# Kernel tuning notes

Hardware: AMD Instinct MI355X
Metric: run time of the kernel (lower is better)

The kernel has to match this reference:

```python
import jax, jax.numpy as jnp
import numpy as np

B, L, EMB, U, V = 128, 64, 512, 1024, 50257
BN_EPS = 0.001


def setup_inputs() -> dict:
    key = jax.random.key(0)
    ks = jax.random.split(key, 20)
    s = 0.02
    return {
        "x": jax.random.randint(ks[0], (B, 1), 0, V, dtype=jnp.int64),
        "features": jax.random.normal(ks[1], (B, L, EMB), jnp.float32),
        "hidden": jax.random.normal(ks[2], (1, B, U), jnp.float32),
        "emb_table": jax.random.normal(ks[3], (V, EMB), jnp.float32) * s,
        "Uattn_w": jax.random.normal(ks[4], (U, EMB), jnp.float32) * s,
        "Uattn_b": jnp.zeros((U,), jnp.float32),
        "Wattn_w": jax.random.normal(ks[5], (U, U), jnp.float32) * s,
        "Wattn_b": jnp.zeros((U,), jnp.float32),
        "Vattn_w": jax.random.normal(ks[6], (1, U), jnp.float32) * s,
        "Vattn_b": jnp.zeros((1,), jnp.float32),
        "W_ih": jax.random.normal(ks[7], (3 * U, U), jnp.float32) * s,
        "W_hh": jax.random.normal(ks[8], (3 * U, U), jnp.float32) * s,
        "b_ih": jnp.zeros((3 * U,), jnp.float32),
        "b_hh": jnp.zeros((3 * U,), jnp.float32),
        "fc_w": jax.random.normal(ks[9], (U, U), jnp.float32) * s,
        "fc_b": jnp.zeros((U,), jnp.float32),
        "bn_gamma": jnp.ones((U,), jnp.float32),
        "bn_beta": jnp.zeros((U,), jnp.float32),
        "bn_mean": jnp.zeros((U,), jnp.float32),
        "bn_var": jnp.ones((U,), jnp.float32),
        "fc2_w": jax.random.normal(ks[10], (V, U), jnp.float32) * s,
        "fc2_b": jnp.zeros((V,), jnp.float32),
    }


def reference(x, features, hidden, emb_table, Uattn_w, Uattn_b, Wattn_w, Wattn_b,
              Vattn_w, Vattn_b, W_ih, W_hh, b_ih, b_hh, fc_w, fc_b,
              bn_gamma, bn_beta, bn_mean, bn_var, fc2_w, fc2_b):
    h = hidden[0]  # [B, U]
    # Bahdanau attention
    Uf = jnp.einsum('ble,ue->blu', features, Uattn_w) + Uattn_b        # [B,L,U]
    Wh = h @ Wattn_w.T + Wattn_b                                        # [B,U]
    score = jnp.tanh(Uf + Wh[:, None, :]) @ Vattn_w.T + Vattn_b        # [B,L,1]
    attn = jax.nn.softmax(score, axis=1)                                # [B,L,1]
    ctx = jnp.sum(attn * features, axis=1)                              # [B,EMB]
    # embed token and concat -> GRU input (seq len 1)
    e = emb_table[x[:, 0]]                                              # [B,EMB]
    gin = jnp.concatenate([ctx, e], axis=-1)                            # [B,U]
    # single-step GRU (PyTorch gate convention)
    gi = gin @ W_ih.T + b_ih                                            # [B,3U]
    gh = h @ W_hh.T + b_hh                                              # [B,3U]
    i_r, i_z, i_n = jnp.split(gi, 3, axis=-1)
    h_r, h_z, h_n = jnp.split(gh, 3, axis=-1)
    r = jax.nn.sigmoid(i_r + h_r)
    z = jax.nn.sigmoid(i_z + h_z)
    n = jnp.tanh(i_n + r * h_n)
    h_new = (1.0 - z) * n + z * h                                       # [B,U]
    # head: fc -> (dropout: identity in eval) -> BN (eval) -> fc2
    y = h_new @ fc_w.T + fc_b
    y = (y - bn_mean) * jax.lax.rsqrt(bn_var + BN_EPS) * bn_gamma + bn_beta
    logits = y @ fc2_w.T + fc2_b                                        # [B,V]
    return logits, h_new[None, :, :], attn
```

## Files before the change

### kernel.cpp

```cpp
#include <hip/hip_runtime.h>

typedef short bf8 __attribute__((ext_vector_type(8)));
typedef float f32x4 __attribute__((ext_vector_type(4)));

__device__ inline short f2bfs(float f) {
    unsigned u = __builtin_bit_cast(unsigned, f);
    u += 0x7FFFu + ((u >> 16) & 1u);
    return (short)(u >> 16);
}

__device__ inline unsigned pk2(float x, float y) {
    return (unsigned)(unsigned short)f2bfs(x) |
           ((unsigned)(unsigned short)f2bfs(y) << 16);
}

__device__ inline float bf2f(short s) {
    unsigned u = ((unsigned)(unsigned short)s) << 16;
    return __builtin_bit_cast(float, u);
}

__device__ inline bf8 cvt_frag(f32x4 lo, f32x4 hi) {
    union { bf8 v; unsigned u[4]; } r;
    r.u[0] = pk2(lo[0], lo[1]);
    r.u[1] = pk2(lo[2], lo[3]);
    r.u[2] = pk2(hi[0], hi[1]);
    r.u[3] = pk2(hi[2], hi[3]);
    return r.v;
}

__device__ inline void gl_lds16(const void* g, void* l) {
    __builtin_amdgcn_global_load_lds(
        (const __attribute__((address_space(1))) unsigned int*)g,
        (__attribute__((address_space(3))) unsigned int*)l,
        16, 0, 0);
}

#define BAR() asm volatile("s_barrier" ::: "memory")

template<int N> __device__ __forceinline__ void waitvm() {
    if constexpr (N == 8)      asm volatile("s_waitcnt vmcnt(8)"  ::: "memory");
    else if constexpr (N == 6) asm volatile("s_waitcnt vmcnt(6)"  ::: "memory");
    else if constexpr (N == 4) asm volatile("s_waitcnt vmcnt(4)"  ::: "memory");
    else if constexpr (N == 3) asm volatile("s_waitcnt vmcnt(3)"  ::: "memory");
    else                       asm volatile("s_waitcnt vmcnt(0)"  ::: "memory");
}

#define MFMA16 __builtin_amdgcn_mfma_f32_16x16x32_bf16

template<int EPI, int BM_, bool OBF>
__device__ __forceinline__ void gemm_body(
    char* smem,
    const short* __restrict__ A, const float* __restrict__ W,
    const float* __restrict__ bias, void* __restrict__ Cv,
    int N, int K, int lda, int n0, int m0,
    const float* __restrict__ q0, const float* __restrict__ q1,
    const float* __restrict__ q2, const float* __restrict__ q3,
    float* __restrict__ score)
{
    constexpr int FM  = BM_ / 32;
    constexpr int ATS = BM_ * 64;
    constexpr int LPT = (BM_ == 128) ? 4 : 3;

    const int lane = threadIdx.x & 63;
    const int wave = threadIdx.x >> 6;
    const int wm0  = (wave >> 1) * (BM_ / 2);
    const int wn0  = (wave & 1) * 32;
    const int lr   = lane & 15;
    const int g    = lane >> 4;

    f32x4 acc[FM][2] = {};

    auto stage = [&](int buf, int k0) {
        char* sA = smem + buf * ATS;
        char* sW = smem + 3 * ATS + buf * 8192;
        #pragma unroll
        for (int cc = 0; cc < BM_ / 64; ++cc) {
            int c  = wave * (BM_ / 64) + cc;
            int r  = c * 16 + (lane >> 2);
            int ss = (lane & 3) ^ ((r >> 1) & 3);
            gl_lds16(&A[(size_t)(m0 + r) * lda + k0 + ss * 8], sA + c * 1024);
        }
        #pragma unroll
        for (int cc = 0; cc < 2; ++cc) {
            int c  = wave * 2 + cc;
            int r  = c * 8 + (lane >> 3);
            int ss = (lane & 7) ^ (r & 7);
            int rg = n0 + r; rg = rg < N ? rg : N - 1;
            gl_lds16(&W[(size_t)rg * K + k0 + ss * 4], sW + c * 1024);
        }
    };

    auto compute = [&](int buf) {
        char* sA = smem + buf * ATS;
        char* sW = smem + 3 * ATS + buf * 8192;
        bf8 av[FM], bv[2];
        #pragma unroll
        for (int i = 0; i < FM; ++i) {
            int ra = wm0 + i * 16 + lr;
            int sl = g ^ ((ra >> 1) & 3);
            av[i] = *reinterpret_cast<const bf8*>(sA + ra * 64 + sl * 16);
        }
        #pragma unroll
        for (int j = 0; j < 2; ++j) {
            int rb = wn0 + j * 16 + lr;
            int l0 = (2 * g)     ^ (rb & 7);
            int l1 = (2 * g + 1) ^ (rb & 7);
            f32x4 lo = *reinterpret_cast<const f32x4*>(sW + rb * 128 + l0 * 16);
            f32x4 hi = *reinterpret_cast<const f32x4*>(sW + rb * 128 + l1 * 16);
            bv[j] = cvt_frag(lo, hi);
        }
        #pragma unroll
        for (int i = 0; i < FM; ++i)
            #pragma unroll
            for (int j = 0; j < 2; ++j)
                acc[i][j] = MFMA16(av[i], bv[j], acc[i][j], 0, 0, 0);
    };

    const int nt = K >> 5;
    stage(0, 0); stage(1, 32);
    int bs = 2, bc = 0;
    for (int t = 0; t < nt - 2; ++t) {
        stage(bs, (t + 2) << 5);
        bs = (bs == 2) ? 0 : bs + 1;
        waitvm<2 * LPT>(); BAR();
        compute(bc);
        bc = (bc == 2) ? 0 : bc + 1;
        BAR();
    }
    waitvm<1 * LPT>(); BAR(); compute(bc); bc = (bc == 2) ? 0 : bc + 1; BAR();
    waitvm<0>();       BAR(); compute(bc);

    if constexpr (EPI == 2) {
        #pragma unroll
        for (int i = 0; i < FM; ++i) {
            #pragma unroll
            for (int r = 0; r < 4; ++r) {
                int m = m0 + wm0 + i * 16 + g * 4 + r;
                int bidx = m >> 6;
                float s = 0.f;
                #pragma unroll
                for (int j = 0; j < 2; ++j) {
                    int n = n0 + wn0 + j * 16 + lr;
                    s += tanhf(acc[i][j][r] + bias[n] + q0[(size_t)bidx * N + n]) * q1[n];
                }
                #pragma unroll
                for (int off = 1; off < 16; off <<= 1)
                    s += __shfl_xor(s, off);
                if (lr == 0) atomicAdd(&score[m], s);
            }
        }
    } else {
        #pragma unroll
        for (int j = 0; j < 2; ++j) {
            int n = n0 + wn0 + j * 16 + lr;
            if (n >= N) continue;
            float bn_ = bias[n];
            float sc = 1.f, sh = 0.f;
            if constexpr (EPI == 1) {
                sc = q0[n] * rsqrtf(q3[n] + 1e-3f);
                sh = q1[n] - q2[n] * sc;
            }
            #pragma unroll
            for (int i = 0; i < FM; ++i) {
                #pragma unroll
                for (int r = 0; r < 4; ++r) {
                    int m = m0 + wm0 + i * 16 + g * 4 + r;
                    float v = acc[i][j][r] + bn_;
                    if constexpr (EPI == 1) v = v * sc + sh;
                    if constexpr (OBF) ((short*)Cv)[(size_t)m * N + n] = f2bfs(v);
                    else               ((float*)Cv)[(size_t)m * N + n] = v;
                }
            }
        }
    }
}

template<int EPI, int BM_, bool OBF>
__global__ __launch_bounds__(256) void gemm_k(
    const short* __restrict__ A, const float* __restrict__ W,
    const float* __restrict__ bias, void* __restrict__ Cv,
    int N, int K, int lda,
    const float* __restrict__ q0, const float* __restrict__ q1,
    const float* __restrict__ q2, const float* __restrict__ q3,
    float* __restrict__ score)
{
    __shared__ __align__(1024) char smem[3 * BM_ * 64 + 3 * 8192];
    gemm_body<EPI, BM_, OBF>(smem, A, W, bias, Cv, N, K, lda,
                             blockIdx.x * 64, blockIdx.y * BM_,
                             q0, q1, q2, q3, score);
}

__global__ __launch_bounds__(256) void gemm_dual(
    const short* __restrict__ A0, const float* __restrict__ W0,
    const float* __restrict__ b0, float* __restrict__ C0,
    const short* __restrict__ A1, const float* __restrict__ W1,
    const float* __restrict__ b1, float* __restrict__ C1,
    int N, int K, int lda)
{
    __shared__ __align__(1024) char smem[3 * 64 * 64 + 3 * 8192];
    if (blockIdx.z == 0)
        gemm_body<0, 64, false>(smem, A0, W0, b0, C0, N, K, lda,
                                blockIdx.x * 64, blockIdx.y * 64,
                                nullptr, nullptr, nullptr, nullptr, nullptr);
    else
        gemm_body<0, 64, false>(smem, A1, W1, b1, C1, N, K, lda,
                                blockIdx.x * 64, blockIdx.y * 64,
                                nullptr, nullptr, nullptr, nullptr, nullptr);
}

__global__ __launch_bounds__(256) void prep_all(
    const float* __restrict__ feat, short* __restrict__ feat_bf,
    const float* __restrict__ h, short* __restrict__ h_bf,
    float* __restrict__ score, const float* __restrict__ vb)
{
    int t = blockIdx.x * 256 + threadIdx.x;
    {
        float4 v0 = *reinterpret_cast<const float4*>(feat + (size_t)t * 8);
        float4 v1 = *reinterpret_cast<const float4*>(feat + (size_t)t * 8 + 4);
        uint4 q = make_uint4(pk2(v0.x, v0.y), pk2(v0.z, v0.w),
                             pk2(v1.x, v1.y), pk2(v1.z, v1.w));
        *reinterpret_cast<uint4*>(feat_bf + (size_t)t * 8) = q;
    }
    if (t < 16384) {
        float4 v0 = *reinterpret_cast<const float4*>(h + (size_t)t * 8);
        float4 v1 = *reinterpret_cast<const float4*>(h + (size_t)t * 8 + 4);
        uint4 q = make_uint4(pk2(v0.x, v0.y), pk2(v0.z, v0.w),
                             pk2(v1.x, v1.y), pk2(v1.z, v1.w));
        *reinterpret_cast<uint4*>(h_bf + (size_t)t * 8) = q;
    }
    if (t < 1024) {
        float v = vb[0];
        float4 vv = make_float4(v, v, v, v);
        *reinterpret_cast<float4*>(score + t * 8)     = vv;
        *reinterpret_cast<float4*>(score + t * 8 + 4) = vv;
    }
}

__global__ __launch_bounds__(256) void softmax_ctx(
    const float* __restrict__ score, const short* __restrict__ feat_bf,
    const int* __restrict__ x, const float* __restrict__ emb,
    float* __restrict__ attn_out, short* __restrict__ gin_bf)
{
    int b = blockIdx.x;
    int t = threadIdx.x;
    __shared__ float sa[64];
    if (t < 64) {
        float v = score[b * 64 + t];
        float m = v;
        #pragma unroll
        for (int off = 32; off; off >>= 1) m = fmaxf(m, __shfl_xor(m, off));
        float e = expf(v - m);
        float s = e;
        #pragma unroll
        for (int off = 32; off; off >>= 1) s += __shfl_xor(s, off);
        float a = e / s;
        attn_out[b * 64 + t] = a;
        sa[t] = a;
    }
    __syncthreads();
    {
        int e0 = t * 2;
        float c0 = 0.f, c1 = 0.f;
        #pragma unroll 4
        for (int l = 0; l < 64; ++l) {
            float a = sa[l];
            unsigned v = *reinterpret_cast<const unsigned*>(
                &feat_bf[((size_t)b * 64 + l) * 512 + e0]);
            c0 += a * bf2f((short)(v & 0xffff));
            c1 += a * bf2f((short)(v >> 16));
        }
        *reinterpret_cast<unsigned*>(&gin_bf[(size_t)b * 1024 + e0]) = pk2(c0, c1);
    }
    {
        int xi = x[b];
        int e0 = t * 2;
        float2 ev = *reinterpret_cast<const float2*>(&emb[(size_t)xi * 512 + e0]);
        *reinterpret_cast<unsigned*>(&gin_bf[(size_t)b * 1024 + 512 + e0]) = pk2(ev.x, ev.y);
    }
}

__global__ __launch_bounds__(256) void gru_kernel(
    const float* __restrict__ gi, const float* __restrict__ gh,
    const float* __restrict__ h, float* __restrict__ hnew,
    short* __restrict__ hnew_bf)
{
    int idx = blockIdx.x * 256 + threadIdx.x;
    int b = idx >> 10, u = idx & 1023;
    const float* gib = gi + (size_t)b * 3072;
    const float* ghb = gh + (size_t)b * 3072;
    float ir = gib[u], iz = gib[1024 + u], in_ = gib[2048 + u];
    float hr = ghb[u], hz = ghb[1024 + u], hn = ghb[2048 + u];
    float r = 1.f / (1.f + expf(-(ir + hr)));
    float z = 1.f / (1.f + expf(-(iz + hz)));
    float n = tanhf(in_ + r * hn);
    float val = (1.f - z) * n + z * h[idx];
    hnew[idx] = val;
    hnew_bf[idx] = f2bfs(val);
}

extern "C" void kernel_launch(void* const* d_in, const int* in_sizes, int n_in,
                              void* d_out, int out_size, void* d_ws, size_t ws_size,
                              hipStream_t stream)
{
    const int*   x        = (const int*)  d_in[0];
    const float* features = (const float*)d_in[1];
    const float* hidden   = (const float*)d_in[2];
    const float* emb      = (const float*)d_in[3];
    const float* Uattn_w  = (const float*)d_in[4];
    const float* Uattn_b  = (const float*)d_in[5];
    const float* Wattn_w  = (const float*)d_in[6];
    const float* Wattn_b  = (const float*)d_in[7];
    const float* Vattn_w  = (const float*)d_in[8];
    const float* Vattn_b  = (const float*)d_in[9];
    const float* W_ih     = (const float*)d_in[10];
    const float* W_hh     = (const float*)d_in[11];
    const float* b_ih     = (const float*)d_in[12];
    const float* b_hh     = (const float*)d_in[13];
    const float* fc_w     = (const float*)d_in[14];
    const float* fc_b     = (const float*)d_in[15];
    const float* bn_gamma = (const float*)d_in[16];
    const float* bn_beta  = (const float*)d_in[17];
    const float* bn_mean  = (const float*)d_in[18];
    const float* bn_var   = (const float*)d_in[19];
    const float* fc2_w    = (const float*)d_in[20];
    const float* fc2_b    = (const float*)d_in[21];

    float* out    = (float*)d_out;
    float* logits = out;
    float* hnew   = out + 6432896;
    float* attn   = out + 6432896 + 131072;

    float* ws        = (float*)d_ws;
    float* Wh        = ws;
    float* scoreb    = ws + 131072;
    float* gi        = ws + 139264;
    float* gh        = ws + 532480;
    short* hidden_bf = (short*)(ws + 925696);
    short* gin_bf    = (short*)(ws + 991232);
    short* hnew_bf   = (short*)(ws + 1056768);
    short* y_bf      = (short*)(ws + 1122304);
    short* feat_bf   = (short*)(ws + 1187840);

    prep_all<<<2048, 256, 0, stream>>>(features, feat_bf, hidden, hidden_bf,
                                       scoreb, Vattn_b);

    gemm_k<0, 64, false><<<dim3(16, 2), 256, 0, stream>>>(
        hidden_bf, Wattn_w, Wattn_b, Wh, 1024, 1024, 1024,
        nullptr, nullptr, nullptr, nullptr, nullptr);

    gemm_k<2, 128, false><<<dim3(16, 64), 256, 0, stream>>>(
        feat_bf, Uattn_w, Uattn_b, nullptr, 1024, 512, 512,
        Wh, Vattn_w, nullptr, nullptr, scoreb);

    softmax_ctx<<<128, 256, 0, stream>>>(scoreb, feat_bf, x, emb, attn, gin_bf);

    gemm_dual<<<dim3(48, 2, 2), 256, 0, stream>>>(
        gin_bf, W_ih, b_ih, gi,
        hidden_bf, W_hh, b_hh, gh, 3072, 1024, 1024);

    gru_kernel<<<512, 256, 0, stream>>>(gi, gh, hidden, hnew, hnew_bf);

    gemm_k<1, 64, true><<<dim3(16, 2), 256, 0, stream>>>(
        hnew_bf, fc_w, fc_b, y_bf, 1024, 1024, 1024,
        bn_gamma, bn_beta, bn_mean, bn_var, nullptr);

    gemm_k<0, 128, false><<<dim3(786, 1), 256, 0, stream>>>(
        y_bf, fc2_w, fc2_b, logits, 50257, 1024, 1024,
        nullptr, nullptr, nullptr, nullptr, nullptr);
}
```

Measured before the change: 153.7 us.

## Fuse Wh GEMM into prep, read fp32 activations directly, specialize fc2 GEMM

Adds an fp32-A path to the GEMM body so hidden and h_new are converted to bf16 in LDS, removing the separate hidden_bf and hnew_bf buffers. The Wattn GEMM is folded into the prep kernel as extra blocks, which removes one launch. A dedicated fc2 kernel loads A fragments straight from global memory into registers and stages only W in LDS, with a 4-blocks-per-CU occupancy hint. tanh and exp are replaced with fast approximations, which adds small numerical error.

```diff
diff --git a/kernel.cpp b/kernel.cpp
--- a/kernel.cpp
+++ b/kernel.cpp
@@ -28,6 +28,12 @@
     return r.v;
 }
 
+__device__ inline float fast_tanh(float x) {
+    x = fminf(fmaxf(x, -15.f), 15.f);
+    float e = __expf(2.f * x);
+    return (e - 1.f) / (e + 1.f);
+}
+
 __device__ inline void gl_lds16(const void* g, void* l) {
     __builtin_amdgcn_global_load_lds(
         (const __attribute__((address_space(1))) unsigned int*)g,
@@ -38,7 +44,8 @@
 #define BAR() asm volatile("s_barrier" ::: "memory")
 
 template<int N> __device__ __forceinline__ void waitvm() {
-    if constexpr (N == 8)      asm volatile("s_waitcnt vmcnt(8)"  ::: "memory");
+    if constexpr (N == 12)     asm volatile("s_waitcnt vmcnt(12)" ::: "memory");
+    else if constexpr (N == 8) asm volatile("s_waitcnt vmcnt(8)"  ::: "memory");
     else if constexpr (N == 6) asm volatile("s_waitcnt vmcnt(6)"  ::: "memory");
     else if constexpr (N == 4) asm volatile("s_waitcnt vmcnt(4)"  ::: "memory");
     else if constexpr (N == 3) asm volatile("s_waitcnt vmcnt(3)"  ::: "memory");
@@ -47,10 +54,10 @@
 
 #define MFMA16 __builtin_amdgcn_mfma_f32_16x16x32_bf16
 
-template<int EPI, int BM_, bool OBF>
+template<int EPI, int BM_, bool OBF, bool AF32>
 __device__ __forceinline__ void gemm_body(
     char* smem,
-    const short* __restrict__ A, const float* __restrict__ W,
+    const void* __restrict__ Av, const float* __restrict__ W,
     const float* __restrict__ bias, void* __restrict__ Cv,
     int N, int K, int lda, int n0, int m0,
     const float* __restrict__ q0, const float* __restrict__ q1,
@@ -58,8 +65,8 @@
     float* __restrict__ score)
 {
     constexpr int FM  = BM_ / 32;
-    constexpr int ATS = BM_ * 64;
-    constexpr int LPT = (BM_ == 128) ? 4 : 3;
+    constexpr int ATS = AF32 ? BM_ * 128 : BM_ * 64;
+    constexpr int LPT = (AF32 ? BM_ / 32 : BM_ / 64) + 2;
 
     const int lane = threadIdx.x & 63;
     const int wave = threadIdx.x >> 6;
@@ -73,12 +80,24 @@
     auto stage = [&](int buf, int k0) {
         char* sA = smem + buf * ATS;
         char* sW = smem + 3 * ATS + buf * 8192;
-        #pragma unroll
-        for (int cc = 0; cc < BM_ / 64; ++cc) {
-            int c  = wave * (BM_ / 64) + cc;
-            int r  = c * 16 + (lane >> 2);
-            int ss = (lane & 3) ^ ((r >> 1) & 3);
-            gl_lds16(&A[(size_t)(m0 + r) * lda + k0 + ss * 8], sA + c * 1024);
+        if constexpr (!AF32) {
+            const short* A = (const short*)Av;
+            #pragma unroll
+            for (int cc = 0; cc < BM_ / 64; ++cc) {
+                int c  = wave * (BM_ / 64) + cc;
+                int r  = c * 16 + (lane >> 2);
+                int ss = (lane & 3) ^ ((r >> 1) & 3);
+                gl_lds16(&A[(size_t)(m0 + r) * lda + k0 + ss * 8], sA + c * 1024);
+            }
+        } else {
+            const float* A = (const float*)Av;
+            #pragma unroll
+            for (int cc = 0; cc < BM_ / 32; ++cc) {
+                int c  = wave * (BM_ / 32) + cc;
+                int r  = c * 8 + (lane >> 3);
+                int ss = (lane & 7) ^ (r & 7);
+                gl_lds16(&A[(size_t)(m0 + r) * lda + k0 + ss * 4], sA + c * 1024);
+            }
         }
         #pragma unroll
         for (int cc = 0; cc < 2; ++cc) {
@@ -97,8 +116,16 @@
         #pragma unroll
         for (int i = 0; i < FM; ++i) {
             int ra = wm0 + i * 16 + lr;
-            int sl = g ^ ((ra >> 1) & 3);
-            av[i] = *reinterpret_cast<const bf8*>(sA + ra * 64 + sl * 16);
+            if constexpr (!AF32) {
+                int sl = g ^ ((ra >> 1) & 3);
+                av[i] = *reinterpret_cast<const bf8*>(sA + ra * 64 + sl * 16);
+            } else {
+                int l0 = (2 * g)     ^ (ra & 7);
+                int l1 = (2 * g + 1) ^ (ra & 7);
+                f32x4 lo = *reinterpret_cast<const f32x4*>(sA + ra * 128 + l0 * 16);
+                f32x4 hi = *reinterpret_cast<const f32x4*>(sA + ra * 128 + l1 * 16);
+                av[i] = cvt_frag(lo, hi);
+            }
         }
         #pragma unroll
         for (int j = 0; j < 2; ++j) {
@@ -141,7 +168,7 @@
                 #pragma unroll
                 for (int j = 0; j < 2; ++j) {
                     int n = n0 + wn0 + j * 16 + lr;
-                    s += tanhf(acc[i][j][r] + bias[n] + q0[(size_t)bidx * N + n]) * q1[n];
+                    s += fast_tanh(acc[i][j][r] + bias[n] + q0[(size_t)bidx * N + n]) * q1[n];
                 }
                 #pragma unroll
                 for (int off = 1; off < 16; off <<= 1)
@@ -175,64 +202,159 @@
     }
 }
 
-template<int EPI, int BM_, bool OBF>
+template<int EPI, int BM_, bool OBF, bool AF32>
 __global__ __launch_bounds__(256) void gemm_k(
-    const short* __restrict__ A, const float* __restrict__ W,
+    const void* __restrict__ A, const float* __restrict__ W,
     const float* __restrict__ bias, void* __restrict__ Cv,
     int N, int K, int lda,
     const float* __restrict__ q0, const float* __restrict__ q1,
     const float* __restrict__ q2, const float* __restrict__ q3,
     float* __restrict__ score)
 {
-    __shared__ __align__(1024) char smem[3 * BM_ * 64 + 3 * 8192];
-    gemm_body<EPI, BM_, OBF>(smem, A, W, bias, Cv, N, K, lda,
-                             blockIdx.x * 64, blockIdx.y * BM_,
-                             q0, q1, q2, q3, score);
+    constexpr int ATS = AF32 ? BM_ * 128 : BM_ * 64;
+    __shared__ __align__(1024) char smem[3 * ATS + 3 * 8192];
+    gemm_body<EPI, BM_, OBF, AF32>(smem, A, W, bias, Cv, N, K, lda,
+                                   blockIdx.x * 64, blockIdx.y * BM_,
+                                   q0, q1, q2, q3, score);
 }
 
 __global__ __launch_bounds__(256) void gemm_dual(
     const short* __restrict__ A0, const float* __restrict__ W0,
     const float* __restrict__ b0, float* __restrict__ C0,
-    const short* __restrict__ A1, const float* __restrict__ W1,
+    const float* __restrict__ A1, const float* __restrict__ W1,
     const float* __restrict__ b1, float* __restrict__ C1,
     int N, int K, int lda)
 {
-    __shared__ __align__(1024) char smem[3 * 64 * 64 + 3 * 8192];
+    __shared__ __align__(1024) char smem[3 * 64 * 128 + 3 * 8192];
     if (blockIdx.z == 0)
-        gemm_body<0, 64, false>(smem, A0, W0, b0, C0, N, K, lda,
-                                blockIdx.x * 64, blockIdx.y * 64,
-                                nullptr, nullptr, nullptr, nullptr, nullptr);
+        gemm_body<0, 64, false, false>(smem, A0, W0, b0, C0, N, K, lda,
+                                       blockIdx.x * 64, blockIdx.y * 64,
+                                       nullptr, nullptr, nullptr, nullptr, nullptr);
     else
-        gemm_body<0, 64, false>(smem, A1, W1, b1, C1, N, K, lda,
-                                blockIdx.x * 64, blockIdx.y * 64,
-                                nullptr, nullptr, nullptr, nullptr, nullptr);
-}
-
-__global__ __launch_bounds__(256) void prep_all(
+        gemm_body<0, 64, false, true>(smem, A1, W1, b1, C1, N, K, lda,
+                                      blockIdx.x * 64, blockIdx.y * 64,
+                                      nullptr, nullptr, nullptr, nullptr, nullptr);
+}
+
+__global__ __launch_bounds__(256, 4) void gemm_fc2(
+    const short* __restrict__ A, const float* __restrict__ W,
+    const float* __restrict__ bias, float* __restrict__ C,
+    int N, int K)
+{
+    __shared__ __align__(1024) char smem[3 * 8192];
+    const int lane = threadIdx.x & 63;
+    const int wave = threadIdx.x >> 6;
+    const int wm0  = (wave >> 1) * 64;
+    const int wn0  = (wave & 1) * 32;
+    const int lr   = lane & 15;
+    const int g    = lane >> 4;
+    const int n0   = blockIdx.x * 64;
+
+    f32x4 acc[4][2] = {};
+
+    const short* Ar0 = A + (size_t)(wm0 +  0 + lr) * K + g * 8;
+    const short* Ar1 = A + (size_t)(wm0 + 16 + lr) * K + g * 8;
+    const short* Ar2 = A + (size_t)(wm0 + 32 + lr) * K + g * 8;
+    const short* Ar3 = A + (size_t)(wm0 + 48 + lr) * K + g * 8;
+
+    auto stageW = [&](int buf, int k0) {
+        char* sW = smem + buf * 8192;
+        #pragma unroll
+        for (int cc = 0; cc < 2; ++cc) {
+            int c  = wave * 2 + cc;
+            int r  = c * 8 + (lane >> 3);
+            int ss = (lane & 7) ^ (r & 7);
+            int rg = n0 + r; rg = rg < N ? rg : N - 1;
+            gl_lds16(&W[(size_t)rg * K + k0 + ss * 4], sW + c * 1024);
+        }
+    };
+    auto loadA = [&](bf8 (&s)[4], int k0) {
+        s[0] = *reinterpret_cast<const bf8*>(Ar0 + k0);
+        s[1] = *reinterpret_cast<const bf8*>(Ar1 + k0);
+        s[2] = *reinterpret_cast<const bf8*>(Ar2 + k0);
+        s[3] = *reinterpret_cast<const bf8*>(Ar3 + k0);
+    };
+    auto computeW = [&](int buf, bf8 (&av)[4]) {
+        char* sW = smem + buf * 8192;
+        bf8 bv[2];
+        #pragma unroll
+        for (int j = 0; j < 2; ++j) {
+            int rb = wn0 + j * 16 + lr;
+            int l0 = (2 * g)     ^ (rb & 7);
+            int l1 = (2 * g + 1) ^ (rb & 7);
+            f32x4 lo = *reinterpret_cast<const f32x4*>(sW + rb * 128 + l0 * 16);
+            f32x4 hi = *reinterpret_cast<const f32x4*>(sW + rb * 128 + l1 * 16);
+            bv[j] = cvt_frag(lo, hi);
+        }
+        #pragma unroll
+        for (int i = 0; i < 4; ++i)
+            #pragma unroll
+            for (int j = 0; j < 2; ++j)
+                acc[i][j] = MFMA16(av[i], bv[j], acc[i][j], 0, 0, 0);
+    };
+
+    bf8 aA[4], aB[4];
+    const int nt = K >> 5;
+    stageW(0, 0);  loadA(aA, 0);
+    stageW(1, 32); loadA(aB, 32);
+    int bs = 2, bc = 0;
+    for (int t = 0; t < nt - 2; t += 2) {
+        stageW(bs, (t + 2) << 5); bs = (bs == 2) ? 0 : bs + 1;
+        waitvm<8>(); BAR();
+        computeW(bc, aA); bc = (bc == 2) ? 0 : bc + 1;
+        loadA(aA, (t + 2) << 5);
+        BAR();
+        stageW(bs, (t + 3) << 5); bs = (bs == 2) ? 0 : bs + 1;
+        waitvm<8>(); BAR();
+        computeW(bc, aB); bc = (bc == 2) ? 0 : bc + 1;
+        loadA(aB, (t + 3) << 5);
+        BAR();
+    }
+    waitvm<6>(); BAR(); computeW(bc, aA); bc = (bc == 2) ? 0 : bc + 1; BAR();
+    waitvm<0>(); BAR(); computeW(bc, aB);
+
+    #pragma unroll
+    for (int j = 0; j < 2; ++j) {
+        int n = n0 + wn0 + j * 16 + lr;
+        if (n >= N) continue;
+        float bn_ = bias[n];
+        #pragma unroll
+        for (int i = 0; i < 4; ++i) {
+            #pragma unroll
+            for (int r = 0; r < 4; ++r) {
+                int m = wm0 + i * 16 + g * 4 + r;
+                C[(size_t)m * N + n] = acc[i][j][r] + bn_;
+            }
+        }
+    }
+}
+
+__global__ __launch_bounds__(256) void prep_wh(
     const float* __restrict__ feat, short* __restrict__ feat_bf,
-    const float* __restrict__ h, short* __restrict__ h_bf,
-    float* __restrict__ score, const float* __restrict__ vb)
-{
-    int t = blockIdx.x * 256 + threadIdx.x;
-    {
+    float* __restrict__ score, const float* __restrict__ vb,
+    const float* __restrict__ hidden, const float* __restrict__ Wattn_w,
+    const float* __restrict__ Wattn_b, float* __restrict__ Wh)
+{
+    __shared__ __align__(1024) char smem[3 * 64 * 128 + 3 * 8192];
+    if (blockIdx.x < 2048) {
+        int t = blockIdx.x * 256 + threadIdx.x;
         float4 v0 = *reinterpret_cast<const float4*>(feat + (size_t)t * 8);
         float4 v1 = *reinterpret_cast<const float4*>(feat + (size_t)t * 8 + 4);
         uint4 q = make_uint4(pk2(v0.x, v0.y), pk2(v0.z, v0.w),
                              pk2(v1.x, v1.y), pk2(v1.z, v1.w));
         *reinterpret_cast<uint4*>(feat_bf + (size_t)t * 8) = q;
-    }
-    if (t < 16384) {
-        float4 v0 = *reinterpret_cast<const float4*>(h + (size_t)t * 8);
-        float4 v1 = *reinterpret_cast<const float4*>(h + (size_t)t * 8 + 4);
-        uint4 q = make_uint4(pk2(v0.x, v0.y), pk2(v0.z, v0.w),
-                             pk2(v1.x, v1.y), pk2(v1.z, v1.w));
-        *reinterpret_cast<uint4*>(h_bf + (size_t)t * 8) = q;
-    }
-    if (t < 1024) {
-        float v = vb[0];
-        float4 vv = make_float4(v, v, v, v);
-        *reinterpret_cast<float4*>(score + t * 8)     = vv;
-        *reinterpret_cast<float4*>(score + t * 8 + 4) = vv;
+        if (t < 1024) {
+            float v = vb[0];
+            float4 vv = make_float4(v, v, v, v);
+            *reinterpret_cast<float4*>(score + t * 8)     = vv;
+            *reinterpret_cast<float4*>(score + t * 8 + 4) = vv;
+        }
+    } else {
+        int b = blockIdx.x - 2048;
+        gemm_body<0, 64, false, true>(smem, hidden, Wattn_w, Wattn_b, Wh,
+                                      1024, 1024, 1024,
+                                      (b & 15) * 64, (b >> 4) * 64,
+                                      nullptr, nullptr, nullptr, nullptr, nullptr);
     }
 }
 
@@ -249,7 +371,7 @@
         float m = v;
         #pragma unroll
         for (int off = 32; off; off >>= 1) m = fmaxf(m, __shfl_xor(m, off));
-        float e = expf(v - m);
+        float e = __expf(v - m);
         float s = e;
         #pragma unroll
         for (int off = 32; off; off >>= 1) s += __shfl_xor(s, off);
@@ -281,8 +403,7 @@
 
 __global__ __launch_bounds__(256) void gru_kernel(
     const float* __restrict__ gi, const float* __restrict__ gh,
-    const float* __restrict__ h, float* __restrict__ hnew,
-    short* __restrict__ hnew_bf)
+    const float* __restrict__ h, float* __restrict__ hnew)
 {
     int idx = blockIdx.x * 256 + threadIdx.x;
     int b = idx >> 10, u = idx & 1023;
@@ -290,12 +411,10 @@
     const float* ghb = gh + (size_t)b * 3072;
     float ir = gib[u], iz = gib[1024 + u], in_ = gib[2048 + u];
     float hr = ghb[u], hz = ghb[1024 + u], hn = ghb[2048 + u];
-    float r = 1.f / (1.f + expf(-(ir + hr)));
-    float z = 1.f / (1.f + expf(-(iz + hz)));
-    float n = tanhf(in_ + r * hn);
-    float val = (1.f - z) * n + z * h[idx];
-    hnew[idx] = val;
-    hnew_bf[idx] = f2bfs(val);
+    float r = 1.f / (1.f + __expf(-(ir + hr)));
+    float z = 1.f / (1.f + __expf(-(iz + hz)));
+    float n = fast_tanh(in_ + r * hn);
+    hnew[idx] = (1.f - z) * n + z * h[idx];
 }
 
 extern "C" void kernel_launch(void* const* d_in, const int* in_sizes, int n_in,
@@ -330,25 +449,19 @@
     float* hnew   = out + 6432896;
     float* attn   = out + 6432896 + 131072;
 
-    float* ws        = (float*)d_ws;
-    float* Wh        = ws;
-    float* scoreb    = ws + 131072;
-    float* gi        = ws + 139264;
-    float* gh        = ws + 532480;
-    short* hidden_bf = (short*)(ws + 925696);
-    short* gin_bf    = (short*)(ws + 991232);
-    short* hnew_bf   = (short*)(ws + 1056768);
-    short* y_bf      = (short*)(ws + 1122304);
-    short* feat_bf   = (short*)(ws + 1187840);
-
-    prep_all<<<2048, 256, 0, stream>>>(features, feat_bf, hidden, hidden_bf,
-                                       scoreb, Vattn_b);
-
-    gemm_k<0, 64, false><<<dim3(16, 2), 256, 0, stream>>>(
-        hidden_bf, Wattn_w, Wattn_b, Wh, 1024, 1024, 1024,
-        nullptr, nullptr, nullptr, nullptr, nullptr);
-
-    gemm_k<2, 128, false><<<dim3(16, 64), 256, 0, stream>>>(
+    float* ws     = (float*)d_ws;
+    float* Wh     = ws;
+    float* scoreb = ws + 131072;
+    float* gi     = ws + 139264;
+    float* gh     = ws + 532480;
+    short* gin_bf = (short*)(ws + 925696);
+    short* y_bf   = (short*)(ws + 991232);
+    short* feat_bf= (short*)(ws + 1056768);
+
+    prep_wh<<<2080, 256, 0, stream>>>(features, feat_bf, scoreb, Vattn_b,
+                                      hidden, Wattn_w, Wattn_b, Wh);
+
+    gemm_k<2, 128, false, false><<<dim3(16, 64), 256, 0, stream>>>(
         feat_bf, Uattn_w, Uattn_b, nullptr, 1024, 512, 512,
         Wh, Vattn_w, nullptr, nullptr, scoreb);
 
@@ -356,15 +469,13 @@
 
     gemm_dual<<<dim3(48, 2, 2), 256, 0, stream>>>(
         gin_bf, W_ih, b_ih, gi,
-        hidden_bf, W_hh, b_hh, gh, 3072, 1024, 1024);
-
-    gru_kernel<<<512, 256, 0, stream>>>(gi, gh, hidden, hnew, hnew_bf);
-
-    gemm_k<1, 64, true><<<dim3(16, 2), 256, 0, stream>>>(
-        hnew_bf, fc_w, fc_b, y_bf, 1024, 1024, 1024,
+        hidden, W_hh, b_hh, gh, 3072, 1024, 1024);
+
+    gru_kernel<<<512, 256, 0, stream>>>(gi, gh, hidden, hnew);
+
+    gemm_k<1, 64, true, true><<<dim3(16, 2), 256, 0, stream>>>(
+        hnew, fc_w, fc_b, y_bf, 1024, 1024, 1024,
         bn_gamma, bn_beta, bn_mean, bn_var, nullptr);
 
-    gemm_k<0, 128, false><<<dim3(786, 1), 256, 0, stream>>>(
-        y_bf, fc2_w, fc2_b, logits, 50257, 1024, 1024,
-        nullptr, nullptr, nullptr, nullptr, nullptr);
-}
+    gemm_fc2<<<786, 256, 0, stream>>>(y_bf, fc2_w, fc2_b, logits, 50257, 1024);
+}
```

After: 186.4 us. 21.2% more time.
